# Optimization experiments

Measured on AMD Instinct MI355X. Metric: run time of the kernel, lower is better.

Reference implementation:

```python
import jax, jax.numpy as jnp
import numpy as np

SOS_TOKEN = 1


def gru_cell(x, h, Wih, Whh, bih, bhh):
    # torch.nn.GRU gate math; x:[B,H], h:[B,H]; Wih/Whh:[3H,H]
    gi = x @ Wih.T + bih
    gh = h @ Whh.T + bhh
    ir, iz, inn = jnp.split(gi, 3, axis=-1)
    hr, hz, hn = jnp.split(gh, 3, axis=-1)
    r = jax.nn.sigmoid(ir + hr)
    z = jax.nn.sigmoid(iz + hz)
    n = jnp.tanh(inn + r * hn)
    return (1.0 - z) * n + z * h


def setup_inputs() -> dict:
    key = jax.random.key(0)
    ks = jax.random.split(key, 20)
    B, S, T, V, H = 32, 512, 128, 32000, 512
    sc = 0.08
    p = lambda i, shape: (jax.random.normal(ks[i], shape, jnp.float32) * sc)
    return {
        "input_seq": jax.random.randint(ks[0], (B, S), 0, V),
        "target_seq": jax.random.randint(ks[1], (B, T), 0, V),
        "emb": p(2, (V, H)),
        "ef_Wih": p(3, (3 * H, H)), "ef_Whh": p(4, (3 * H, H)),
        "ef_bih": p(5, (3 * H,)), "ef_bhh": p(6, (3 * H,)),
        "eb_Wih": p(7, (3 * H, H)), "eb_Whh": p(8, (3 * H, H)),
        "eb_bih": p(9, (3 * H,)), "eb_bhh": p(10, (3 * H,)),
        "d_Wih": p(11, (3 * H, H)), "d_Whh": p(12, (3 * H, H)),
        "d_bih": p(13, (3 * H,)), "d_bhh": p(14, (3 * H,)),
        "att_W": p(15, (H, 2 * H)), "att_b": p(16, (H,)),
        "out_W": p(17, (V, H)), "out_b": p(18, (V,)),
    }


def reference(input_seq, target_seq, emb,
              ef_Wih, ef_Whh, ef_bih, ef_bhh,
              eb_Wih, eb_Whh, eb_bih, eb_bhh,
              d_Wih, d_Whh, d_bih, d_bhh,
              att_W, att_b, out_W, out_b):
    B, S = input_seq.shape
    T = target_seq.shape[1]
    H = emb.shape[1]
    dtype = emb.dtype

    # ---- encoder: bidirectional GRU over source ----
    xs = jnp.swapaxes(emb[input_seq], 0, 1)  # [S,B,H]
    h0 = jnp.zeros((B, H), dtype)

    def make_step(Wih, Whh, bih, bhh):
        def f(h, xt):
            hn = gru_cell(xt, h, Wih, Whh, bih, bhh)
            return hn, hn
        return f

    hf_last, out_f = jax.lax.scan(make_step(ef_Wih, ef_Whh, ef_bih, ef_bhh), h0, xs)
    hb_last, out_bwd = jax.lax.scan(make_step(eb_Wih, eb_Whh, eb_bih, eb_bhh), h0, xs[::-1])
    out_bwd = out_bwd[::-1]
    # encoder_output[:, :H] + encoder_output[:, H:]  == sum of directions
    enc_out = jnp.swapaxes(out_f + out_bwd, 0, 1)  # [B,S,H]
    # decoder_hidden = encoder_hidden[-1,0] + encoder_hidden[-1,1]
    h_dec0 = hf_last + hb_last  # [B,H]

    # ---- greedy decode for T steps with argmax feedback ----
    tgt = target_seq.T  # [T,B]
    tok0 = jnp.full((B,), SOS_TOKEN, target_seq.dtype)
    batch_idx = jnp.arange(B)

    def dec_step(carry, tgt_t):
        h, tok, loss = carry
        xt = emb[tok]                                   # [B,H]
        hn = gru_cell(xt, h, d_Wih, d_Whh, d_bih, d_bhh)
        scores = jnp.einsum('bh,bsh->bs', hn, enc_out)  # dot attention
        w = jax.nn.softmax(scores, axis=-1)
        ctx = jnp.einsum('bs,bsh->bh', w, enc_out)
        att_out = jnp.tanh(jnp.concatenate([ctx, hn], axis=-1) @ att_W.T + att_b)
        logits = att_out @ out_W.T + out_b              # [B,V]
        logp = jax.nn.log_softmax(logits, axis=-1)
        loss = loss - logp[batch_idx, tgt_t]            # -log softmax(output)[target]
        nxt = jnp.argmax(logits, axis=-1).astype(tok.dtype)
        return (hn, nxt, loss), None

    init = (h_dec0, tok0, jnp.zeros((B,), dtype))
    (_, _, loss), _ = jax.lax.scan(dec_step, init, tgt)
    # mean over examples of (per-example loss / decoding_cnt)
    return jnp.mean(loss / T)
```

## Files before the change

kernel.cpp:

```cpp
#include <hip/hip_runtime.h>
#include <math.h>

#define B 32
#define S 512
#define T 128
#define V 32000
#define H 512
#define NB 256
#define NTE 512
#define NTD 256
#define LCHUNK 250
#define LROWS 128
#define XPITCH 520

__device__ __forceinline__ float dot4(float acc, float4 a, float4 b){
    return fmaf(a.x,b.x, fmaf(a.y,b.y, fmaf(a.z,b.z, fmaf(a.w,b.w, acc))));
}
__device__ __forceinline__ float sigmoidf_(float x){ return 1.0f/(1.0f+expf(-x)); }

template<int GRPSZ>
__device__ __forceinline__ void gbar_arrive(unsigned* bb, unsigned grp, unsigned n){
    __syncthreads();
    if (threadIdx.x == 0){
        const unsigned r = __hip_atomic_fetch_add(bb + grp*32, 1u,
                              __ATOMIC_RELEASE, __HIP_MEMORY_SCOPE_AGENT);
        if (r == n*(unsigned)GRPSZ - 1u){
            const unsigned q = __hip_atomic_fetch_add(bb + 256, 1u,
                                  __ATOMIC_RELEASE, __HIP_MEMORY_SCOPE_AGENT);
            if (q == n*8u - 1u)
                __hip_atomic_store(bb + 288, n,
                                   __ATOMIC_RELEASE, __HIP_MEMORY_SCOPE_AGENT);
        }
    }
}
__device__ __forceinline__ void gbar_wait(unsigned* bb, unsigned n){
    if (threadIdx.x == 0){
        long guard = 0;
        while (__hip_atomic_load(bb + 288, __ATOMIC_RELAXED, __HIP_MEMORY_SCOPE_AGENT) < n){
            __builtin_amdgcn_s_sleep(2);
            if (++guard > 200000000L) break;
        }
        (void)__hip_atomic_load(bb + 288, __ATOMIC_ACQUIRE, __HIP_MEMORY_SCOPE_AGENT);
    }
    __syncthreads();
}

__global__ __launch_bounds__(NTE, 1) void enc_persistent(
    const int* __restrict__ input_seq, const float* __restrict__ emb,
    const float* __restrict__ fWih, const float* __restrict__ fWhh,
    const float* __restrict__ fbih, const float* __restrict__ fbhh,
    const float* __restrict__ bWih, const float* __restrict__ bWhh,
    const float* __restrict__ bbih, const float* __restrict__ bbhh,
    float* enc_out, float* out_b, unsigned* bars)
{
    __shared__ float wlds[24*512];
    __shared__ float shp[3*128*6];
    __shared__ float xh[32*XPITCH];
    const int bk = blockIdx.x, tid = threadIdx.x;
    const int dir = bk & 1, jg = bk >> 1;
    const int b = tid & 31, jj = (tid>>5)&3, kh = tid>>7;
    const int j = jg*4 + jj;
    const unsigned grp = ((unsigned)jg) & 7u;

    const float *Wih = dir? bWih : fWih;
    const float *Whh = dir? bWhh : fWhh;
    const float *bih = dir? bbih : fbih;
    const float *bhh = dir? bbhh : fbhh;
    float* outp = dir? out_b : enc_out;
    unsigned* bar = bars + dir*1024;

    for (int r=0;r<24;r++){
        const int jr = jg*4 + (r/6);
        const int g  = r % 6;
        const float* src = (g<3) ? (Wih + ((size_t)g*H + jr)*H)
                                 : (Whh + ((size_t)(g-3)*H + jr)*H);
        for (int k=tid;k<H;k+=NTE) wlds[r*512+k] = src[k];
    }
    __syncthreads();

    const float4* wx0 = (const float4*)(wlds + (jj*6+0)*512 + kh*128);
    const float4* wx1 = (const float4*)(wlds + (jj*6+1)*512 + kh*128);
    const float4* wx2 = (const float4*)(wlds + (jj*6+2)*512 + kh*128);
    const float4* wh0 = (const float4*)(wlds + (jj*6+3)*512 + kh*128);
    const float4* wh1 = (const float4*)(wlds + (jj*6+4)*512 + kh*128);
    const float4* wh2 = (const float4*)(wlds + (jj*6+5)*512 + kh*128);
    const float bi_r = bih[j], bi_z = bih[H+j], bi_n = bih[2*H+j];
    const float bh_r = bhh[j], bh_z = bhh[H+j], bh_n = bhh[2*H+j];

    for (int t=0; t<S; t++){
        const int pos  = dir ? (S-1-t) : t;
        const int hpos = dir ? (S-t)   : (t-1);

        #pragma unroll
        for (int it=0; it<8; ++it){
            const int idx = it*NTE + tid;
            const int bb = idx >> 7, c = idx & 127;
            const int tok = input_seq[bb*S + pos];
            ((float4*)(xh + bb*XPITCH))[c] =
                ((const float4*)(emb + (size_t)tok*H))[c];
        }
        __syncthreads();

        float ir=0.f, iz=0.f, in_=0.f;
        {
            const float4* x4 = (const float4*)(xh + b*XPITCH + kh*128);
            #pragma unroll 8
            for (int k=0;k<32;k++){
                const float4 xv = x4[k];
                ir  = dot4(ir , xv, wx0[k]);
                iz  = dot4(iz , xv, wx1[k]);
                in_ = dot4(in_, xv, wx2[k]);
            }
        }

        if (t > 0) gbar_wait(bar, (unsigned)t);

        float hr=0.f, hz=0.f, hn=0.f, hprev = 0.f;
        if (t > 0){
            #pragma unroll
            for (int it=0; it<8; ++it){
                const int idx = it*NTE + tid;
                const int bb = idx >> 7, c = idx & 127;
                ((float4*)(xh + bb*XPITCH))[c] =
                    ((const float4*)(outp + ((size_t)bb*S + hpos)*H))[c];
            }
            __syncthreads();
            const float4* h4 = (const float4*)(xh + b*XPITCH + kh*128);
            #pragma unroll 8
            for (int k=0;k<32;k++){
                const float4 hv = h4[k];
                hr = dot4(hr, hv, wh0[k]);
                hz = dot4(hz, hv, wh1[k]);
                hn = dot4(hn, hv, wh2[k]);
            }
            hprev = xh[b*XPITCH + j];
        }
        if (kh){
            float* p = shp + ((kh-1)*128 + jj*32 + b)*6;
            p[0]=ir; p[1]=iz; p[2]=in_; p[3]=hr; p[4]=hz; p[5]=hn;
        }
        __syncthreads();
        if (!kh){
            #pragma unroll
            for (int q=0;q<3;q++){
                const float* p = shp + (q*128 + jj*32 + b)*6;
                ir+=p[0]; iz+=p[1]; in_+=p[2]; hr+=p[3]; hz+=p[4]; hn+=p[5];
            }
            const float r = sigmoidf_(ir + bi_r + hr + bh_r);
            const float z = sigmoidf_(iz + bi_z + hz + bh_z);
            const float n = tanhf(in_ + bi_n + r*(hn + bh_n));
            outp[((size_t)b*S + pos)*H + j] = (1.0f - z)*n + z*hprev;
        }
        gbar_arrive<16>(bar, grp, (unsigned)(t+1));
    }
}

__global__ __launch_bounds__(NTD, 1) void dec_persistent(
    const int* __restrict__ target_seq, const float* __restrict__ emb,
    const float* __restrict__ dWih, const float* __restrict__ dWhh,
    const float* __restrict__ dbih, const float* __restrict__ dbhh,
    const float* __restrict__ attW, const float* __restrict__ attb,
    const float* __restrict__ outW, const float* __restrict__ outBias,
    float* enc_out, const float* out_b,
    float* hdec, float* scores, float* ctxb, float* att_out,
    float* pm, float* ps, int* pidx, float* lossb,
    float* out, unsigned* bar)
{
    __shared__ __align__(16) float smem[128*33*4];
    __shared__ float wg[12*512];
    __shared__ float wp[2*1024];
    __shared__ float red_m[4][32], red_s[4][32];
    __shared__ int   red_i[4][32];
    __shared__ int sh_tok[B];
    const int bk = blockIdx.x, tid = threadIdx.x;
    const unsigned grp = (unsigned)bk & 7u;
    unsigned bn = 1;
#define GSYNC() do { gbar_arrive<32>(bar, grp, bn); gbar_wait(bar, bn); ++bn; } while(0)

    for (int r=0;r<12;r++){
        const int jr = bk*2 + (r/6);
        const int g  = r % 6;
        const float* src = (g<3) ? (dWih + ((size_t)g*H + jr)*H)
                                 : (dWhh + ((size_t)(g-3)*H + jr)*H);
        for (int k=tid;k<H;k+=NTD) wg[r*512+k] = src[k];
    }
    for (int r=0;r<2;r++){
        const float* src = attW + (size_t)(bk*2+r)*(2*H);
        for (int k=tid;k<2*H;k+=NTD) wp[r*1024+k] = src[k];
    }

    {
        const int gid = bk*NTD + tid;
        if (gid < B*H){
            const int bb = gid >> 9, jq = gid & 511;
            hdec[gid] = enc_out[((size_t)bb*S + (S-1))*H + jq] + out_b[((size_t)bb*S)*H + jq];
        }
        if (bk==0 && tid<B) lossb[tid] = 0.0f;
    }
    GSYNC();

    {
        float4* e4 = (float4*)enc_out; const float4* o4 = (const float4*)out_b;
        for (size_t i = (size_t)bk*NTD + tid; i < (size_t)B*S*H/4; i += (size_t)NB*NTD){
            float4 x = e4[i]; const float4 y = o4[i];
            x.x+=y.x; x.y+=y.y; x.z+=y.z; x.w+=y.w; e4[i]=x;
        }
    }
    GSYNC();

    const int gb = tid & 31, gj = (tid>>5)&1, gkq = tid>>6;
    const int jrow = bk*2 + gj;
    const float4* gwir = (const float4*)(wg + (gj*6+0)*512 + gkq*128);
    const float4* gwiz = (const float4*)(wg + (gj*6+1)*512 + gkq*128);
    const float4* gwin = (const float4*)(wg + (gj*6+2)*512 + gkq*128);
    const float4* gwhr = (const float4*)(wg + (gj*6+3)*512 + gkq*128);
    const float4* gwhz = (const float4*)(wg + (gj*6+4)*512 + gkq*128);
    const float4* gwhn = (const float4*)(wg + (gj*6+5)*512 + gkq*128);
    const float gbi_r = dbih[jrow], gbi_z = dbih[H+jrow], gbi_n = dbih[2*H+jrow];
    const float gbh_r = dbhh[jrow], gbh_z = dbhh[H+jrow], gbh_n = dbhh[2*H+jrow];
    const float4* pw = (const float4*)(wp + gj*1024 + gkq*256);

    for (int t=0; t<T; t++){
        float* hin  = hdec + (size_t)(t&1)*B*H;
        float* hout = hdec + (size_t)((t+1)&1)*B*H;

        if (t == 0){
            if (tid < B) sh_tok[tid] = 1;
        } else {
            const int mb = tid>>3, p = tid&7;
            float bv = -INFINITY; int ai = 0x7FFFFFFF;
            for (int c=p; c<LCHUNK; c+=8){
                const float v = pm[mb*LCHUNK + c];
                if (v > bv){ bv = v; ai = pidx[mb*LCHUNK + c]; }
            }
            #pragma unroll
            for (int m=1; m<8; m<<=1){
                const float ov = __shfl_xor(bv, m); const int oi = __shfl_xor(ai, m);
                if (ov > bv || (ov == bv && oi < ai)){ bv = ov; ai = oi; }
            }
            if (p==0) sh_tok[mb] = ai;
            if (bk == 0){
                float mm = -INFINITY;
                for (int c=p; c<LCHUNK; c+=8) mm = fmaxf(mm, pm[mb*LCHUNK+c]);
                #pragma unroll
                for (int m=1;m<8;m<<=1) mm = fmaxf(mm, __shfl_xor(mm, m));
                float se = 0.0f;
                for (int c=p; c<LCHUNK; c+=8) se += ps[mb*LCHUNK+c]*expf(pm[mb*LCHUNK+c]-mm);
                #pragma unroll
                for (int m=1;m<8;m<<=1) se += __shfl_xor(se, m);
                const int tg = target_seq[mb*T + (t-1)];
                const float4* ar = (const float4*)(att_out + (size_t)mb*H) + p*16;
                const float4* wr = (const float4*)(outW + (size_t)tg*H) + p*16;
                float d = 0.0f;
                #pragma unroll
                for (int k=0;k<16;k++) d = dot4(d, ar[k], wr[k]);
                #pragma unroll
                for (int m=1;m<8;m<<=1) d += __shfl_xor(d, m);
                if (p==0) lossb[mb] += (mm + logf(se)) - (d + outBias[tg]);
            }
        }
        __syncthreads();
        {
            const int tokb = sh_tok[gb];
            const float4* x4 = (const float4*)(emb + (size_t)tokb*H + gkq*128);
            const float4* h4 = (const float4*)(hin + (size_t)gb*H + gkq*128);
            float ir=0.f, iz=0.f, in_=0.f, hr=0.f, hz=0.f, hn=0.f;
            #pragma unroll 4
            for (int k=0;k<32;k++){
                const float4 xv = x4[k], hv = h4[k];
                ir  = dot4(ir , xv, gwir[k]);
                iz  = dot4(iz , xv, gwiz[k]);
                in_ = dot4(in_, xv, gwin[k]);
                hr  = dot4(hr , hv, gwhr[k]);
                hz  = dot4(hz , hv, gwhz[k]);
                hn  = dot4(hn , hv, gwhn[k]);
            }
            if (gkq){
                float* pp = smem + ((gkq-1)*64 + gj*32 + gb)*6;
                pp[0]=ir; pp[1]=iz; pp[2]=in_; pp[3]=hr; pp[4]=hz; pp[5]=hn;
            }
            __syncthreads();
            if (!gkq){
                #pragma unroll
                for (int q=0;q<3;q++){
                    const float* pp = smem + (q*64 + gj*32 + gb)*6;
                    ir+=pp[0]; iz+=pp[1]; in_+=pp[2]; hr+=pp[3]; hz+=pp[4]; hn+=pp[5];
                }
                const float r = sigmoidf_(ir + gbi_r + hr + gbh_r);
                const float z = sigmoidf_(iz + gbi_z + hz + gbh_z);
                const float n = tanhf(in_ + gbi_n + r*(hn + gbh_n));
                const float hprev = hin[(size_t)gb*H + jrow];
                hout[(size_t)gb*H + jrow] = (1.0f - z)*n + z*hprev;
            }
        }
        GSYNC();

        {
            const int bS = bk & 31, sg = bk >> 5;
            if (tid < 128)
                ((float4*)smem)[tid] = ((const float4*)(hout + (size_t)bS*H))[tid];
            __syncthreads();
            const int w = tid >> 6, lane = tid & 63;
            const float4 h0 = ((const float4*)smem)[lane];
            const float4 h1 = ((const float4*)smem)[64 + lane];
            const int sbase = sg*64 + w*16;
            #pragma unroll 4
            for (int i=0;i<16;i+=2){
                const int sA = sbase + i, sB = sA + 1;
                const float4* eA = (const float4*)(enc_out + ((size_t)bS*S + sA)*H);
                const float4* eB = (const float4*)(enc_out + ((size_t)bS*S + sB)*H);
                const float4 a0 = eA[lane], a1 = eA[64+lane];
                const float4 b0 = eB[lane], b1 = eB[64+lane];
                float a = dot4(dot4(0.f, a0, h0), a1, h1);
                float b = dot4(dot4(0.f, b0, h0), b1, h1);
                #pragma unroll
                for (int m=1;m<64;m<<=1){ a += __shfl_xor(a, m); b += __shfl_xor(b, m); }
                if (lane == 0){ scores[bS*S + sA] = a; scores[bS*S + sB] = b; }
            }
        }
        GSYNC();

        {
            const int bC = bk & 31, cg = bk >> 5;
            float* sh_w = smem; float* red = smem + 512; float* part = smem + 768;
            const float s0 = scores[bC*S + tid], s1 = scores[bC*S + tid + 256];
            red[tid] = fmaxf(s0,s1); __syncthreads();
            for (int off=128; off>0; off>>=1){ if (tid<off) red[tid]=fmaxf(red[tid],red[tid+off]); __syncthreads(); }
            const float M = red[0]; __syncthreads();
            const float e0 = expf(s0-M), e1 = expf(s1-M);
            red[tid] = e0+e1; __syncthreads();
            for (int off=128; off>0; off>>=1){ if (tid<off) red[tid]+=red[tid+off]; __syncthreads(); }
            const float inv = 1.0f/red[0];
            __syncthreads();
            sh_w[tid] = e0*inv; sh_w[tid+256] = e1*inv;
            __syncthreads();
            const int col = cg*64 + (tid & 63);
            const int sg2 = tid >> 6;
            const float* Ec = enc_out + (size_t)bC*S*H + col;
            float ac0=0.f, ac1=0.f, ac2=0.f, ac3=0.f;
            #pragma unroll 4
            for (int i=0;i<128;i+=4){
                const int sA = sg2 + 4*i, sB = sA+4, sC = sA+8, sD = sA+12;
                const float vA = Ec[(size_t)sA*H], vB = Ec[(size_t)sB*H];
                const float vC = Ec[(size_t)sC*H], vD = Ec[(size_t)sD*H];
                ac0 = fmaf(sh_w[sA], vA, ac0);
                ac1 = fmaf(sh_w[sB], vB, ac1);
                ac2 = fmaf(sh_w[sC], vC, ac2);
                ac3 = fmaf(sh_w[sD], vD, ac3);
            }
            part[tid] = (ac0+ac1)+(ac2+ac3); __syncthreads();
            if (tid < 64) ctxb[bC*512 + col] = part[tid]+part[tid+64]+part[tid+128]+part[tid+192];
        }
        GSYNC();

        {
            const float* act = (gkq < 2) ? (ctxb + (size_t)gb*512 + gkq*256)
                                         : (hout + (size_t)gb*H + (gkq-2)*256);
            const float4* a4 = (const float4*)act;
            float acc = 0.f;
            #pragma unroll 8
            for (int k=0;k<64;k++) acc = dot4(acc, a4[k], pw[k]);
            if (gkq){
                smem[(gkq-1)*64 + gj*32 + gb] = acc;
            }
            __syncthreads();
            if (!gkq){
                acc += smem[0*64 + gj*32 + gb] + smem[1*64 + gj*32 + gb] + smem[2*64 + gj*32 + gb];
                att_out[(size_t)gb*H + jrow] = tanhf(acc + attb[jrow]);
            }
        }
        GSYNC();

        if (bk < LCHUNK){
            float4* sh4 = (float4*)smem;
            for (int idx = tid; idx < 32*128; idx += NTD){
                const int k4 = idx & 127, bb = idx >> 7;
                sh4[k4*33 + bb] = ((const float4*)att_out)[(size_t)bb*128 + k4];
            }
            __syncthreads();
            const int wid = tid >> 6, lane = tid & 63;
            const int rl = lane & 7, bl = lane >> 3;
            const int r0 = bk*LROWS + wid*32 + rl*4;
            const float4* w0 = (const float4*)(outW + (size_t)(r0+0)*H);
            const float4* w1 = (const float4*)(outW + (size_t)(r0+1)*H);
            const float4* w2 = (const float4*)(outW + (size_t)(r0+2)*H);
            const float4* w3 = (const float4*)(outW + (size_t)(r0+3)*H);
            float acc[4][4];
            #pragma unroll
            for (int i=0;i<4;i++){ acc[i][0]=0.f; acc[i][1]=0.f; acc[i][2]=0.f; acc[i][3]=0.f; }

            float4 A0[4],A1[4],A2[4],A3[4], B0[4],B1[4],B2[4],B3[4];
            #pragma unroll
            for (int kk=0;kk<4;kk++){ A0[kk]=w0[kk]; A1[kk]=w1[kk]; A2[kk]=w2[kk]; A3[kk]=w3[kk]; }
            for (int kc=0; kc<16; kc++){
                const int kbB = kc*8 + 4;
                #pragma unroll
                for (int kk=0;kk<4;kk++){ B0[kk]=w0[kbB+kk]; B1[kk]=w1[kbB+kk]; B2[kk]=w2[kbB+kk]; B3[kk]=w3[kbB+kk]; }
                #pragma unroll
                for (int kk=0;kk<4;kk++){
                    const int k = kc*8 + kk;
                    const float4 a0 = sh4[k*33 + bl*4 + 0];
                    const float4 a1 = sh4[k*33 + bl*4 + 1];
                    const float4 a2 = sh4[k*33 + bl*4 + 2];
                    const float4 a3 = sh4[k*33 + bl*4 + 3];
                    acc[0][0]=dot4(acc[0][0],A0[kk],a0); acc[0][1]=dot4(acc[0][1],A0[kk],a1);
                    acc[0][2]=dot4(acc[0][2],A0[kk],a2); acc[0][3]=dot4(acc[0][3],A0[kk],a3);
                    acc[1][0]=dot4(acc[1][0],A1[kk],a0); acc[1][1]=dot4(acc[1][1],A1[kk],a1);
                    acc[1][2]=dot4(acc[1][2],A1[kk],a2); acc[1][3]=dot4(acc[1][3],A1[kk],a3);
                    acc[2][0]=dot4(acc[2][0],A2[kk],a0); acc[2][1]=dot4(acc[2][1],A2[kk],a1);
                    acc[2][2]=dot4(acc[2][2],A2[kk],a2); acc[2][3]=dot4(acc[2][3],A2[kk],a3);
                    acc[3][0]=dot4(acc[3][0],A3[kk],a0); acc[3][1]=dot4(acc[3][1],A3[kk],a1);
                    acc[3][2]=dot4(acc[3][2],A3[kk],a2); acc[3][3]=dot4(acc[3][3],A3[kk],a3);
                }
                if (kc < 15){
                    const int kbA = kc*8 + 8;
                    #pragma unroll
                    for (int kk=0;kk<4;kk++){ A0[kk]=w0[kbA+kk]; A1[kk]=w1[kbA+kk]; A2[kk]=w2[kbA+kk]; A3[kk]=w3[kbA+kk]; }
                }
                #pragma unroll
                for (int kk=0;kk<4;kk++){
                    const int k = kc*8 + 4 + kk;
                    const float4 a0 = sh4[k*33 + bl*4 + 0];
                    const float4 a1 = sh4[k*33 + bl*4 + 1];
                    const float4 a2 = sh4[k*33 + bl*4 + 2];
                    const float4 a3 = sh4[k*33 + bl*4 + 3];
                    acc[0][0]=dot4(acc[0][0],B0[kk],a0); acc[0][1]=dot4(acc[0][1],B0[kk],a1);
                    acc[0][2]=dot4(acc[0][2],B0[kk],a2); acc[0][3]=dot4(acc[0][3],B0[kk],a3);
                    acc[1][0]=dot4(acc[1][0],B1[kk],a0); acc[1][1]=dot4(acc[1][1],B1[kk],a1);
                    acc[1][2]=dot4(acc[1][2],B1[kk],a2); acc[1][3]=dot4(acc[1][3],B1[kk],a3);
                    acc[2][0]=dot4(acc[2][0],B2[kk],a0); acc[2][1]=dot4(acc[2][1],B2[kk],a1);
                    acc[2][2]=dot4(acc[2][2],B2[kk],a2); acc[2][3]=dot4(acc[2][3],B2[kk],a3);
                    acc[3][0]=dot4(acc[3][0],B3[kk],a0); acc[3][1]=dot4(acc[3][1],B3[kk],a1);
                    acc[3][2]=dot4(acc[3][2],B3[kk],a2); acc[3][3]=dot4(acc[3][3],B3[kk],a3);
                }
            }

            const float bs0 = outBias[r0], bs1 = outBias[r0+1], bs2 = outBias[r0+2], bs3 = outBias[r0+3];
            #pragma unroll
            for (int j=0;j<4;j++){
                const float l0 = acc[0][j]+bs0, l1 = acc[1][j]+bs1, l2 = acc[2][j]+bs2, l3 = acc[3][j]+bs3;
                float M = l0; int bi = r0;
                if (l1 > M){ M=l1; bi=r0+1; }
                if (l2 > M){ M=l2; bi=r0+2; }
                if (l3 > M){ M=l3; bi=r0+3; }
                float Ssum = expf(l0-M)+expf(l1-M)+expf(l2-M)+expf(l3-M);
                #pragma unroll
                for (int m=1;m<8;m<<=1){
                    const float oM = __shfl_xor(M, m);
                    const float oS = __shfl_xor(Ssum, m);
                    const int   oI = __shfl_xor(bi, m);
                    const float nM = fmaxf(M, oM);
                    const float nS = Ssum*expf(M-nM) + oS*expf(oM-nM);
                    if (oM > M || (oM == M && oI < bi)) bi = oI;
                    M = nM; Ssum = nS;
                }
                if (rl == 0){
                    red_m[wid][bl*4+j] = M;
                    red_s[wid][bl*4+j] = Ssum;
                    red_i[wid][bl*4+j] = bi;
                }
            }
            __syncthreads();
            if (tid < 32){
                float M = red_m[0][tid], Ssum = red_s[0][tid]; int bi = red_i[0][tid];
                #pragma unroll
                for (int w=1; w<4; w++){
                    const float oM = red_m[w][tid], oS = red_s[w][tid]; const int oI = red_i[w][tid];
                    const float nM = fmaxf(M, oM);
                    const float nS = Ssum*expf(M-nM) + oS*expf(oM-nM);
                    if (oM > M || (oM == M && oI < bi)) bi = oI;
                    M = nM; Ssum = nS;
                }
                pm[tid*LCHUNK + bk] = M;
                ps[tid*LCHUNK + bk] = Ssum;
                pidx[tid*LCHUNK + bk] = bi;
            }
        }
        GSYNC();
    }

    if (bk == 0){
        const int mb = tid>>3, p = tid&7;
        float mm = -INFINITY;
        for (int c=p; c<LCHUNK; c+=8) mm = fmaxf(mm, pm[mb*LCHUNK+c]);
        #pragma unroll
        for (int m=1;m<8;m<<=1) mm = fmaxf(mm, __shfl_xor(mm, m));
        float se = 0.0f;
        for (int c=p; c<LCHUNK; c+=8) se += ps[mb*LCHUNK+c]*expf(pm[mb*LCHUNK+c]-mm);
        #pragma unroll
        for (int m=1;m<8;m<<=1) se += __shfl_xor(se, m);
        const int tg = target_seq[mb*T + (T-1)];
        const float4* ar = (const float4*)(att_out + (size_t)mb*H) + p*16;
        const float4* wr = (const float4*)(outW + (size_t)tg*H) + p*16;
        float d = 0.0f;
        #pragma unroll
        for (int k=0;k<16;k++) d = dot4(d, ar[k], wr[k]);
        #pragma unroll
        for (int m=1;m<8;m<<=1) d += __shfl_xor(d, m);
        if (p==0) lossb[mb] += (mm + logf(se)) - (d + outBias[tg]);
        __syncthreads();
        if (tid < B){
            float v = lossb[tid];
            for (int off=16; off>0; off>>=1) v += __shfl_down(v, off);
            if (tid == 0) out[0] = v / (float)(B*T);
        }
    }
#undef GSYNC
}

extern "C" void kernel_launch(void* const* d_in, const int* in_sizes, int n_in,
                              void* d_out, int out_size, void* d_ws, size_t ws_size,
                              hipStream_t stream)
{
    const int*   input_seq  = (const int*)  d_in[0];
    const int*   target_seq = (const int*)  d_in[1];
    const float* emb    = (const float*)d_in[2];
    const float* efWih  = (const float*)d_in[3];
    const float* efWhh  = (const float*)d_in[4];
    const float* efbih  = (const float*)d_in[5];
    const float* efbhh  = (const float*)d_in[6];
    const float* ebWih  = (const float*)d_in[7];
    const float* ebWhh  = (const float*)d_in[8];
    const float* ebbih  = (const float*)d_in[9];
    const float* ebbhh  = (const float*)d_in[10];
    const float* dWih   = (const float*)d_in[11];
    const float* dWhh   = (const float*)d_in[12];
    const float* dbih   = (const float*)d_in[13];
    const float* dbhh   = (const float*)d_in[14];
    const float* attW   = (const float*)d_in[15];
    const float* attb   = (const float*)d_in[16];
    const float* outW   = (const float*)d_in[17];
    const float* outBias= (const float*)d_in[18];

    float* ws      = (float*)d_ws;
    unsigned* bars = (unsigned*)ws;
    float* enc_out = ws + 4096;
    float* outb    = enc_out + (size_t)B*S*H;
    float* scores  = outb    + (size_t)B*S*H;
    float* ctxb    = scores  + (size_t)B*S;
    float* attout  = ctxb    + (size_t)B*512;
    float* pm      = attout  + (size_t)B*H;
    float* ps      = pm      + (size_t)B*LCHUNK;
    int*   pidx    = (int*)(ps + (size_t)B*LCHUNK);
    float* hdec    = (float*)(pidx + (size_t)B*LCHUNK);
    float* lossb   = hdec    + (size_t)2*B*H;

    hipMemsetAsync(bars, 0, 16384, stream);

    enc_persistent<<<NB, NTE, 0, stream>>>(input_seq, emb,
        efWih, efWhh, efbih, efbhh, ebWih, ebWhh, ebbih, ebbhh,
        enc_out, outb, bars);

    dec_persistent<<<NB, NTD, 0, stream>>>(target_seq, emb,
        dWih, dWhh, dbih, dbhh, attW, attb, outW, outBias,
        enc_out, outb, hdec, scores, ctxb, attout,
        pm, ps, pidx, lossb, (float*)d_out, bars + 2048);
}
```

Measured before the change: 28.79 ms.

## Double decoder block size to 512 threads and re-partition every phase

Raises the persistent decoder kernel from 256 to 512 threads per block. Each phase (GRU gate dot products, attention scores, softmax/context, attention projection, output-vocab logits) is re-split so every thread does half the K-range or half the rows, with wider shared-memory reductions. The aim is more in-flight memory requests and latency hiding per CU in a latency-bound, barrier-heavy persistent loop. In exchange it adds longer reduction chains and costs more registers per CU.

```diff
diff --git a/kernel.cpp b/kernel.cpp
--- a/kernel.cpp
+++ b/kernel.cpp
@@ -8,7 +8,7 @@
 #define H 512
 #define NB 256
 #define NTE 512
-#define NTD 256
+#define NTD 512
 #define LCHUNK 250
 #define LROWS 128
 #define XPITCH 520
@@ -169,8 +169,8 @@
     __shared__ __align__(16) float smem[128*33*4];
     __shared__ float wg[12*512];
     __shared__ float wp[2*1024];
-    __shared__ float red_m[4][32], red_s[4][32];
-    __shared__ int   red_i[4][32];
+    __shared__ float red_m[8][32], red_s[8][32];
+    __shared__ int   red_i[8][32];
     __shared__ int sh_tok[B];
     const int bk = blockIdx.x, tid = threadIdx.x;
     const unsigned grp = (unsigned)bk & 7u;
@@ -210,15 +210,15 @@
 
     const int gb = tid & 31, gj = (tid>>5)&1, gkq = tid>>6;
     const int jrow = bk*2 + gj;
-    const float4* gwir = (const float4*)(wg + (gj*6+0)*512 + gkq*128);
-    const float4* gwiz = (const float4*)(wg + (gj*6+1)*512 + gkq*128);
-    const float4* gwin = (const float4*)(wg + (gj*6+2)*512 + gkq*128);
-    const float4* gwhr = (const float4*)(wg + (gj*6+3)*512 + gkq*128);
-    const float4* gwhz = (const float4*)(wg + (gj*6+4)*512 + gkq*128);
-    const float4* gwhn = (const float4*)(wg + (gj*6+5)*512 + gkq*128);
+    const float4* gwir = (const float4*)(wg + (gj*6+0)*512 + gkq*64);
+    const float4* gwiz = (const float4*)(wg + (gj*6+1)*512 + gkq*64);
+    const float4* gwin = (const float4*)(wg + (gj*6+2)*512 + gkq*64);
+    const float4* gwhr = (const float4*)(wg + (gj*6+3)*512 + gkq*64);
+    const float4* gwhz = (const float4*)(wg + (gj*6+4)*512 + gkq*64);
+    const float4* gwhn = (const float4*)(wg + (gj*6+5)*512 + gkq*64);
     const float gbi_r = dbih[jrow], gbi_z = dbih[H+jrow], gbi_n = dbih[2*H+jrow];
     const float gbh_r = dbhh[jrow], gbh_z = dbhh[H+jrow], gbh_n = dbhh[2*H+jrow];
-    const float4* pw = (const float4*)(wp + gj*1024 + gkq*256);
+    const float4* pw = (const float4*)(wp + gj*1024 + gkq*128);
 
     for (int t=0; t<T; t++){
         float* hin  = hdec + (size_t)(t&1)*B*H;
@@ -226,7 +226,7 @@
 
         if (t == 0){
             if (tid < B) sh_tok[tid] = 1;
-        } else {
+        } else if (tid < 256) {
             const int mb = tid>>3, p = tid&7;
             float bv = -INFINITY; int ai = 0x7FFFFFFF;
             for (int c=p; c<LCHUNK; c+=8){
@@ -262,11 +262,11 @@
         __syncthreads();
         {
             const int tokb = sh_tok[gb];
-            const float4* x4 = (const float4*)(emb + (size_t)tokb*H + gkq*128);
-            const float4* h4 = (const float4*)(hin + (size_t)gb*H + gkq*128);
+            const float4* x4 = (const float4*)(emb + (size_t)tokb*H + gkq*64);
+            const float4* h4 = (const float4*)(hin + (size_t)gb*H + gkq*64);
             float ir=0.f, iz=0.f, in_=0.f, hr=0.f, hz=0.f, hn=0.f;
-            #pragma unroll 4
-            for (int k=0;k<32;k++){
+            #pragma unroll
+            for (int k=0;k<16;k++){
                 const float4 xv = x4[k], hv = h4[k];
                 ir  = dot4(ir , xv, gwir[k]);
                 iz  = dot4(iz , xv, gwiz[k]);
@@ -282,7 +282,7 @@
             __syncthreads();
             if (!gkq){
                 #pragma unroll
-                for (int q=0;q<3;q++){
+                for (int q=0;q<7;q++){
                     const float* pp = smem + (q*64 + gj*32 + gb)*6;
                     ir+=pp[0]; iz+=pp[1]; in_+=pp[2]; hr+=pp[3]; hz+=pp[4]; hn+=pp[5];
                 }
@@ -303,9 +303,9 @@
             const int w = tid >> 6, lane = tid & 63;
             const float4 h0 = ((const float4*)smem)[lane];
             const float4 h1 = ((const float4*)smem)[64 + lane];
-            const int sbase = sg*64 + w*16;
-            #pragma unroll 4
-            for (int i=0;i<16;i+=2){
+            const int sbase = sg*64 + w*8;
+            #pragma unroll
+            for (int i=0;i<8;i+=2){
                 const int sA = sbase + i, sB = sA + 1;
                 const float4* eA = (const float4*)(enc_out + ((size_t)bS*S + sA)*H);
                 const float4* eB = (const float4*)(enc_out + ((size_t)bS*S + sB)*H);
@@ -322,25 +322,25 @@
 
         {
             const int bC = bk & 31, cg = bk >> 5;
-            float* sh_w = smem; float* red = smem + 512; float* part = smem + 768;
-            const float s0 = scores[bC*S + tid], s1 = scores[bC*S + tid + 256];
-            red[tid] = fmaxf(s0,s1); __syncthreads();
-            for (int off=128; off>0; off>>=1){ if (tid<off) red[tid]=fmaxf(red[tid],red[tid+off]); __syncthreads(); }
+            float* sh_w = smem; float* red = smem + 512; float* part = smem + 1024;
+            const float s0 = scores[bC*S + tid];
+            red[tid] = s0; __syncthreads();
+            for (int off=256; off>0; off>>=1){ if (tid<off) red[tid]=fmaxf(red[tid],red[tid+off]); __syncthreads(); }
             const float M = red[0]; __syncthreads();
-            const float e0 = expf(s0-M), e1 = expf(s1-M);
-            red[tid] = e0+e1; __syncthreads();
-            for (int off=128; off>0; off>>=1){ if (tid<off) red[tid]+=red[tid+off]; __syncthreads(); }
+            const float e0 = expf(s0-M);
+            red[tid] = e0; __syncthreads();
+            for (int off=256; off>0; off>>=1){ if (tid<off) red[tid]+=red[tid+off]; __syncthreads(); }
             const float inv = 1.0f/red[0];
             __syncthreads();
-            sh_w[tid] = e0*inv; sh_w[tid+256] = e1*inv;
+            sh_w[tid] = e0*inv;
             __syncthreads();
             const int col = cg*64 + (tid & 63);
             const int sg2 = tid >> 6;
             const float* Ec = enc_out + (size_t)bC*S*H + col;
             float ac0=0.f, ac1=0.f, ac2=0.f, ac3=0.f;
             #pragma unroll 4
-            for (int i=0;i<128;i+=4){
-                const int sA = sg2 + 4*i, sB = sA+4, sC = sA+8, sD = sA+12;
+            for (int i=0;i<64;i+=4){
+                const int sA = sg2 + 8*i, sB = sA+8, sC = sA+16, sD = sA+24;
                 const float vA = Ec[(size_t)sA*H], vB = Ec[(size_t)sB*H];
                 const float vC = Ec[(size_t)sC*H], vD = Ec[(size_t)sD*H];
                 ac0 = fmaf(sh_w[sA], vA, ac0);
@@ -349,23 +349,29 @@
                 ac3 = fmaf(sh_w[sD], vD, ac3);
             }
             part[tid] = (ac0+ac1)+(ac2+ac3); __syncthreads();
-            if (tid < 64) ctxb[bC*512 + col] = part[tid]+part[tid+64]+part[tid+128]+part[tid+192];
+            if (tid < 64){
+                float v = 0.f;
+                #pragma unroll
+                for (int i=0;i<8;i++) v += part[tid + 64*i];
+                ctxb[bC*512 + cg*64 + tid] = v;
+            }
         }
         GSYNC();
 
         {
-            const float* act = (gkq < 2) ? (ctxb + (size_t)gb*512 + gkq*256)
-                                         : (hout + (size_t)gb*H + (gkq-2)*256);
+            const float* act = (gkq < 4) ? (ctxb + (size_t)gb*512 + gkq*128)
+                                         : (hout + (size_t)gb*H + (gkq-4)*128);
             const float4* a4 = (const float4*)act;
             float acc = 0.f;
-            #pragma unroll 8
-            for (int k=0;k<64;k++) acc = dot4(acc, a4[k], pw[k]);
+            #pragma unroll
+            for (int k=0;k<32;k++) acc = dot4(acc, a4[k], pw[k]);
             if (gkq){
                 smem[(gkq-1)*64 + gj*32 + gb] = acc;
             }
             __syncthreads();
             if (!gkq){
-                acc += smem[0*64 + gj*32 + gb] + smem[1*64 + gj*32 + gb] + smem[2*64 + gj*32 + gb];
+                #pragma unroll
+                for (int q=0;q<7;q++) acc += smem[q*64 + gj*32 + gb];
                 att_out[(size_t)gb*H + jrow] = tanhf(acc + attb[jrow]);
             }
         }
@@ -380,22 +386,20 @@
             __syncthreads();
             const int wid = tid >> 6, lane = tid & 63;
             const int rl = lane & 7, bl = lane >> 3;
-            const int r0 = bk*LROWS + wid*32 + rl*4;
+            const int r0 = bk*LROWS + wid*16 + rl*2;
             const float4* w0 = (const float4*)(outW + (size_t)(r0+0)*H);
             const float4* w1 = (const float4*)(outW + (size_t)(r0+1)*H);
-            const float4* w2 = (const float4*)(outW + (size_t)(r0+2)*H);
-            const float4* w3 = (const float4*)(outW + (size_t)(r0+3)*H);
-            float acc[4][4];
-            #pragma unroll
-            for (int i=0;i<4;i++){ acc[i][0]=0.f; acc[i][1]=0.f; acc[i][2]=0.f; acc[i][3]=0.f; }
-
-            float4 A0[4],A1[4],A2[4],A3[4], B0[4],B1[4],B2[4],B3[4];
-            #pragma unroll
-            for (int kk=0;kk<4;kk++){ A0[kk]=w0[kk]; A1[kk]=w1[kk]; A2[kk]=w2[kk]; A3[kk]=w3[kk]; }
+            float acc[2][4];
+            acc[0][0]=0.f; acc[0][1]=0.f; acc[0][2]=0.f; acc[0][3]=0.f;
+            acc[1][0]=0.f; acc[1][1]=0.f; acc[1][2]=0.f; acc[1][3]=0.f;
+
+            float4 A0[4],A1[4], B0[4],B1[4];
+            #pragma unroll
+            for (int kk=0;kk<4;kk++){ A0[kk]=w0[kk]; A1[kk]=w1[kk]; }
             for (int kc=0; kc<16; kc++){
                 const int kbB = kc*8 + 4;
                 #pragma unroll
-                for (int kk=0;kk<4;kk++){ B0[kk]=w0[kbB+kk]; B1[kk]=w1[kbB+kk]; B2[kk]=w2[kbB+kk]; B3[kk]=w3[kbB+kk]; }
+                for (int kk=0;kk<4;kk++){ B0[kk]=w0[kbB+kk]; B1[kk]=w1[kbB+kk]; }
                 #pragma unroll
                 for (int kk=0;kk<4;kk++){
                     const int k = kc*8 + kk;
@@ -407,15 +411,11 @@
                     acc[0][2]=dot4(acc[0][2],A0[kk],a2); acc[0][3]=dot4(acc[0][3],A0[kk],a3);
                     acc[1][0]=dot4(acc[1][0],A1[kk],a0); acc[1][1]=dot4(acc[1][1],A1[kk],a1);
                     acc[1][2]=dot4(acc[1][2],A1[kk],a2); acc[1][3]=dot4(acc[1][3],A1[kk],a3);
-                    acc[2][0]=dot4(acc[2][0],A2[kk],a0); acc[2][1]=dot4(acc[2][1],A2[kk],a1);
-                    acc[2][2]=dot4(acc[2][2],A2[kk],a2); acc[2][3]=dot4(acc[2][3],A2[kk],a3);
-                    acc[3][0]=dot4(acc[3][0],A3[kk],a0); acc[3][1]=dot4(acc[3][1],A3[kk],a1);
-                    acc[3][2]=dot4(acc[3][2],A3[kk],a2); acc[3][3]=dot4(acc[3][3],A3[kk],a3);
                 }
                 if (kc < 15){
                     const int kbA = kc*8 + 8;
                     #pragma unroll
-                    for (int kk=0;kk<4;kk++){ A0[kk]=w0[kbA+kk]; A1[kk]=w1[kbA+kk]; A2[kk]=w2[kbA+kk]; A3[kk]=w3[kbA+kk]; }
+                    for (int kk=0;kk<4;kk++){ A0[kk]=w0[kbA+kk]; A1[kk]=w1[kbA+kk]; }
                 }
                 #pragma unroll
                 for (int kk=0;kk<4;kk++){
@@ -428,22 +428,16 @@
                     acc[0][2]=dot4(acc[0][2],B0[kk],a2); acc[0][3]=dot4(acc[0][3],B0[kk],a3);
                     acc[1][0]=dot4(acc[1][0],B1[kk],a0); acc[1][1]=dot4(acc[1][1],B1[kk],a1);
                     acc[1][2]=dot4(acc[1][2],B1[kk],a2); acc[1][3]=dot4(acc[1][3],B1[kk],a3);
-                    acc[2][0]=dot4(acc[2][0],B2[kk],a0); acc[2][1]=dot4(acc[2][1],B2[kk],a1);
-                    acc[2][2]=dot4(acc[2][2],B2[kk],a2); acc[2][3]=dot4(acc[2][3],B2[kk],a3);
-                    acc[3][0]=dot4(acc[3][0],B3[kk],a0); acc[3][1]=dot4(acc[3][1],B3[kk],a1);
-                    acc[3][2]=dot4(acc[3][2],B3[kk],a2); acc[3][3]=dot4(acc[3][3],B3[kk],a3);
-                }
-            }
-
-            const float bs0 = outBias[r0], bs1 = outBias[r0+1], bs2 = outBias[r0+2], bs3 = outBias[r0+3];
+                }
+            }
+
+            const float bs0 = outBias[r0], bs1 = outBias[r0+1];
             #pragma unroll
             for (int j=0;j<4;j++){
-                const float l0 = acc[0][j]+bs0, l1 = acc[1][j]+bs1, l2 = acc[2][j]+bs2, l3 = acc[3][j]+bs3;
+                const float l0 = acc[0][j]+bs0, l1 = acc[1][j]+bs1;
                 float M = l0; int bi = r0;
                 if (l1 > M){ M=l1; bi=r0+1; }
-                if (l2 > M){ M=l2; bi=r0+2; }
-                if (l3 > M){ M=l3; bi=r0+3; }
-                float Ssum = expf(l0-M)+expf(l1-M)+expf(l2-M)+expf(l3-M);
+                float Ssum = expf(l0-M)+expf(l1-M);
                 #pragma unroll
                 for (int m=1;m<8;m<<=1){
                     const float oM = __shfl_xor(M, m);
@@ -464,7 +458,7 @@
             if (tid < 32){
                 float M = red_m[0][tid], Ssum = red_s[0][tid]; int bi = red_i[0][tid];
                 #pragma unroll
-                for (int w=1; w<4; w++){
+                for (int w=1; w<8; w++){
                     const float oM = red_m[w][tid], oS = red_s[w][tid]; const int oI = red_i[w][tid];
                     const float nM = fmaxf(M, oM);
                     const float nS = Ssum*expf(M-nM) + oS*expf(oM-nM);
@@ -480,24 +474,26 @@
     }
 
     if (bk == 0){
-        const int mb = tid>>3, p = tid&7;
-        float mm = -INFINITY;
-        for (int c=p; c<LCHUNK; c+=8) mm = fmaxf(mm, pm[mb*LCHUNK+c]);
-        #pragma unroll
-        for (int m=1;m<8;m<<=1) mm = fmaxf(mm, __shfl_xor(mm, m));
-        float se = 0.0f;
-        for (int c=p; c<LCHUNK; c+=8) se += ps[mb*LCHUNK+c]*expf(pm[mb*LCHUNK+c]-mm);
-        #pragma unroll
-        for (int m=1;m<8;m<<=1) se += __shfl_xor(se, m);
-        const int tg = target_seq[mb*T + (T-1)];
-        const float4* ar = (const float4*)(att_out + (size_t)mb*H) + p*16;
-        const float4* wr = (const float4*)(outW + (size_t)tg*H) + p*16;
-        float d = 0.0f;
-        #pragma unroll
-        for (int k=0;k<16;k++) d = dot4(d, ar[k], wr[k]);
-        #pragma unroll
-        for (int m=1;m<8;m<<=1) d += __shfl_xor(d, m);
-        if (p==0) lossb[mb] += (mm + logf(se)) - (d + outBias[tg]);
+        if (tid < 256){
+            const int mb = tid>>3, p = tid&7;
+            float mm = -INFINITY;
+            for (int c=p; c<LCHUNK; c+=8) mm = fmaxf(mm, pm[mb*LCHUNK+c]);
+            #pragma unroll
+            for (int m=1;m<8;m<<=1) mm = fmaxf(mm, __shfl_xor(mm, m));
+            float se = 0.0f;
+            for (int c=p; c<LCHUNK; c+=8) se += ps[mb*LCHUNK+c]*expf(pm[mb*LCHUNK+c]-mm);
+            #pragma unroll
+            for (int m=1;m<8;m<<=1) se += __shfl_xor(se, m);
+            const int tg = target_seq[mb*T + (T-1)];
+            const float4* ar = (const float4*)(att_out + (size_t)mb*H) + p*16;
+            const float4* wr = (const float4*)(outW + (size_t)tg*H) + p*16;
+            float d = 0.0f;
+            #pragma unroll
+            for (int k=0;k<16;k++) d = dot4(d, ar[k], wr[k]);
+            #pragma unroll
+            for (int m=1;m<8;m<<=1) d += __shfl_xor(d, m);
+            if (p==0) lossb[mb] += (mm + logf(se)) - (d + outBias[tg]);
+        }
         __syncthreads();
         if (tid < B){
             float v = lossb[tid];
```

New measurement: 30.20 ms. 1.05x slower.

## Pin a quarter of each block's output-projection weights in LDS

Applied to the files above, without the earlier changes.

Each decoder block now preloads the first 32 of its 128 output-projection rows into shared memory once, and wave 0 reads them from LDS every step while the other waves keep streaming from global memory. To free LDS, the attention-projection weights are no longer cached and are read from global memory each step. The per-batch loss reduction is also spread across blocks (bk==mb) instead of all running in block 0. This trades less global/L2 traffic for the big vocab GEMV against extra global reads for the attention weights and load imbalance between waves.

```diff
diff --git a/kernel.cpp b/kernel.cpp
--- a/kernel.cpp
+++ b/kernel.cpp
@@ -11,6 +11,8 @@
 #define NTD 256
 #define LCHUNK 250
 #define LROWS 128
+#define NPIN 32
+#define PINP 516
 #define XPITCH 520
 
 __device__ __forceinline__ float dot4(float acc, float4 a, float4 b){
@@ -168,7 +170,7 @@
 {
     __shared__ __align__(16) float smem[128*33*4];
     __shared__ float wg[12*512];
-    __shared__ float wp[2*1024];
+    __shared__ __align__(16) float pinw[NPIN*PINP];
     __shared__ float red_m[4][32], red_s[4][32];
     __shared__ int   red_i[4][32];
     __shared__ int sh_tok[B];
@@ -184,9 +186,12 @@
                                  : (dWhh + ((size_t)(g-3)*H + jr)*H);
         for (int k=tid;k<H;k+=NTD) wg[r*512+k] = src[k];
     }
-    for (int r=0;r<2;r++){
-        const float* src = attW + (size_t)(bk*2+r)*(2*H);
-        for (int k=tid;k<2*H;k+=NTD) wp[r*1024+k] = src[k];
+    if (bk < LCHUNK){
+        for (int idx = tid; idx < NPIN*128; idx += NTD){
+            const int row = idx >> 7, k4 = idx & 127;
+            ((float4*)(pinw + row*PINP))[k4] =
+                ((const float4*)(outW + (size_t)(bk*LROWS + row)*H))[k4];
+        }
     }
 
     {
@@ -218,7 +223,7 @@
     const float4* gwhn = (const float4*)(wg + (gj*6+5)*512 + gkq*128);
     const float gbi_r = dbih[jrow], gbi_z = dbih[H+jrow], gbi_n = dbih[2*H+jrow];
     const float gbh_r = dbhh[jrow], gbh_z = dbhh[H+jrow], gbh_n = dbhh[2*H+jrow];
-    const float4* pw = (const float4*)(wp + gj*1024 + gkq*256);
+    const float4* pwG = (const float4*)(attW + (size_t)jrow*(2*H)) + gkq*64;
 
     for (int t=0; t<T; t++){
         float* hin  = hdec + (size_t)(t&1)*B*H;
@@ -239,7 +244,7 @@
                 if (ov > bv || (ov == bv && oi < ai)){ bv = ov; ai = oi; }
             }
             if (p==0) sh_tok[mb] = ai;
-            if (bk == 0){
+            if (bk == mb){
                 float mm = -INFINITY;
                 for (int c=p; c<LCHUNK; c+=8) mm = fmaxf(mm, pm[mb*LCHUNK+c]);
                 #pragma unroll
@@ -359,7 +364,7 @@
             const float4* a4 = (const float4*)act;
             float acc = 0.f;
             #pragma unroll 8
-            for (int k=0;k<64;k++) acc = dot4(acc, a4[k], pw[k]);
+            for (int k=0;k<64;k++) acc = dot4(acc, a4[k], pwG[k]);
             if (gkq){
                 smem[(gkq-1)*64 + gj*32 + gb] = acc;
             }
@@ -381,57 +386,83 @@
             const int wid = tid >> 6, lane = tid & 63;
             const int rl = lane & 7, bl = lane >> 3;
             const int r0 = bk*LROWS + wid*32 + rl*4;
-            const float4* w0 = (const float4*)(outW + (size_t)(r0+0)*H);
-            const float4* w1 = (const float4*)(outW + (size_t)(r0+1)*H);
-            const float4* w2 = (const float4*)(outW + (size_t)(r0+2)*H);
-            const float4* w3 = (const float4*)(outW + (size_t)(r0+3)*H);
             float acc[4][4];
             #pragma unroll
             for (int i=0;i<4;i++){ acc[i][0]=0.f; acc[i][1]=0.f; acc[i][2]=0.f; acc[i][3]=0.f; }
 
-            float4 A0[4],A1[4],A2[4],A3[4], B0[4],B1[4],B2[4],B3[4];
-            #pragma unroll
-            for (int kk=0;kk<4;kk++){ A0[kk]=w0[kk]; A1[kk]=w1[kk]; A2[kk]=w2[kk]; A3[kk]=w3[kk]; }
-            for (int kc=0; kc<16; kc++){
-                const int kbB = kc*8 + 4;
-                #pragma unroll
-                for (int kk=0;kk<4;kk++){ B0[kk]=w0[kbB+kk]; B1[kk]=w1[kbB+kk]; B2[kk]=w2[kbB+kk]; B3[kk]=w3[kbB+kk]; }
-                #pragma unroll
-                for (int kk=0;kk<4;kk++){
-                    const int k = kc*8 + kk;
+            if (wid == 0){
+                const float4* p0 = (const float4*)(pinw + (rl*4+0)*PINP);
+                const float4* p1 = (const float4*)(pinw + (rl*4+1)*PINP);
+                const float4* p2 = (const float4*)(pinw + (rl*4+2)*PINP);
+                const float4* p3 = (const float4*)(pinw + (rl*4+3)*PINP);
+                #pragma unroll 4
+                for (int k=0;k<128;k++){
                     const float4 a0 = sh4[k*33 + bl*4 + 0];
                     const float4 a1 = sh4[k*33 + bl*4 + 1];
                     const float4 a2 = sh4[k*33 + bl*4 + 2];
                     const float4 a3 = sh4[k*33 + bl*4 + 3];
-                    acc[0][0]=dot4(acc[0][0],A0[kk],a0); acc[0][1]=dot4(acc[0][1],A0[kk],a1);
-                    acc[0][2]=dot4(acc[0][2],A0[kk],a2); acc[0][3]=dot4(acc[0][3],A0[kk],a3);
-                    acc[1][0]=dot4(acc[1][0],A1[kk],a0); acc[1][1]=dot4(acc[1][1],A1[kk],a1);
-                    acc[1][2]=dot4(acc[1][2],A1[kk],a2); acc[1][3]=dot4(acc[1][3],A1[kk],a3);
-                    acc[2][0]=dot4(acc[2][0],A2[kk],a0); acc[2][1]=dot4(acc[2][1],A2[kk],a1);
-                    acc[2][2]=dot4(acc[2][2],A2[kk],a2); acc[2][3]=dot4(acc[2][3],A2[kk],a3);
-                    acc[3][0]=dot4(acc[3][0],A3[kk],a0); acc[3][1]=dot4(acc[3][1],A3[kk],a1);
-                    acc[3][2]=dot4(acc[3][2],A3[kk],a2); acc[3][3]=dot4(acc[3][3],A3[kk],a3);
+                    {   const float4 wv = p0[k];
+                        acc[0][0]=dot4(acc[0][0],wv,a0); acc[0][1]=dot4(acc[0][1],wv,a1);
+                        acc[0][2]=dot4(acc[0][2],wv,a2); acc[0][3]=dot4(acc[0][3],wv,a3); }
+                    {   const float4 wv = p1[k];
+                        acc[1][0]=dot4(acc[1][0],wv,a0); acc[1][1]=dot4(acc[1][1],wv,a1);
+                        acc[1][2]=dot4(acc[1][2],wv,a2); acc[1][3]=dot4(acc[1][3],wv,a3); }
+                    {   const float4 wv = p2[k];
+                        acc[2][0]=dot4(acc[2][0],wv,a0); acc[2][1]=dot4(acc[2][1],wv,a1);
+                        acc[2][2]=dot4(acc[2][2],wv,a2); acc[2][3]=dot4(acc[2][3],wv,a3); }
+                    {   const float4 wv = p3[k];
+                        acc[3][0]=dot4(acc[3][0],wv,a0); acc[3][1]=dot4(acc[3][1],wv,a1);
+                        acc[3][2]=dot4(acc[3][2],wv,a2); acc[3][3]=dot4(acc[3][3],wv,a3); }
                 }
-                if (kc < 15){
-                    const int kbA = kc*8 + 8;
+            } else {
+                const float4* w0 = (const float4*)(outW + (size_t)(r0+0)*H);
+                const float4* w1 = (const float4*)(outW + (size_t)(r0+1)*H);
+                const float4* w2 = (const float4*)(outW + (size_t)(r0+2)*H);
+                const float4* w3 = (const float4*)(outW + (size_t)(r0+3)*H);
+                float4 A0[4],A1[4],A2[4],A3[4], B0[4],B1[4],B2[4],B3[4];
+                #pragma unroll
+                for (int kk=0;kk<4;kk++){ A0[kk]=w0[kk]; A1[kk]=w1[kk]; A2[kk]=w2[kk]; A3[kk]=w3[kk]; }
+                for (int kc=0; kc<16; kc++){
+                    const int kbB = kc*8 + 4;
                     #pragma unroll
-                    for (int kk=0;kk<4;kk++){ A0[kk]=w0[kbA+kk]; A1[kk]=w1[kbA+kk]; A2[kk]=w2[kbA+kk]; A3[kk]=w3[kbA+kk]; }
-                }
-                #pragma unroll
-                for (int kk=0;kk<4;kk++){
-                    const int k = kc*8 + 4 + kk;
-                    const float4 a0 = sh4[k*33 + bl*4 + 0];
-                    const float4 a1 = sh4[k*33 + bl*4 + 1];
-                    const float4 a2 = sh4[k*33 + bl*4 + 2];
-                    const float4 a3 = sh4[k*33 + bl*4 + 3];
-                    acc[0][0]=dot4(acc[0][0],B0[kk],a0); acc[0][1]=dot4(acc[0][1],B0[kk],a1);
-                    acc[0][2]=dot4(acc[0][2],B0[kk],a2); acc[0][3]=dot4(acc[0][3],B0[kk],a3);
-                    acc[1][0]=dot4(acc[1][0],B1[kk],a0); acc[1][1]=dot4(acc[1][1],B1[kk],a1);
-                    acc[1][2]=dot4(acc[1][2],B1[kk],a2); acc[1][3]=dot4(acc[1][3],B1[kk],a3);
-                    acc[2][0]=dot4(acc[2][0],B2[kk],a0); acc[2][1]=dot4(acc[2][1],B2[kk],a1);
-                    acc[2][2]=dot4(acc[2][2],B2[kk],a2); acc[2][3]=dot4(acc[2][3],B2[kk],a3);
-                    acc[3][0]=dot4(acc[3][0],B3[kk],a0); acc[3][1]=dot4(acc[3][1],B3[kk],a1);
-                    acc[3][2]=dot4(acc[3][2],B3[kk],a2); acc[3][3]=dot4(acc[3][3],B3[kk],a3);
+                    for (int kk=0;kk<4;kk++){ B0[kk]=w0[kbB+kk]; B1[kk]=w1[kbB+kk]; B2[kk]=w2[kbB+kk]; B3[kk]=w3[kbB+kk]; }
+                    #pragma unroll
+                    for (int kk=0;kk<4;kk++){
+                        const int k = kc*8 + kk;
+                        const float4 a0 = sh4[k*33 + bl*4 + 0];
+                        const float4 a1 = sh4[k*33 + bl*4 + 1];
+                        const float4 a2 = sh4[k*33 + bl*4 + 2];
+                        const float4 a3 = sh4[k*33 + bl*4 + 3];
+                        acc[0][0]=dot4(acc[0][0],A0[kk],a0); acc[0][1]=dot4(acc[0][1],A0[kk],a1);
+                        acc[0][2]=dot4(acc[0][2],A0[kk],a2); acc[0][3]=dot4(acc[0][3],A0[kk],a3);
+                        acc[1][0]=dot4(acc[1][0],A1[kk],a0); acc[1][1]=dot4(acc[1][1],A1[kk],a1);
+                        acc[1][2]=dot4(acc[1][2],A1[kk],a2); acc[1][3]=dot4(acc[1][3],A1[kk],a3);
+                        acc[2][0]=dot4(acc[2][0],A2[kk],a0); acc[2][1]=dot4(acc[2][1],A2[kk],a1);
+                        acc[2][2]=dot4(acc[2][2],A2[kk],a2); acc[2][3]=dot4(acc[2][3],A2[kk],a3);
+                        acc[3][0]=dot4(acc[3][0],A3[kk],a0); acc[3][1]=dot4(acc[3][1],A3[kk],a1);
+                        acc[3][2]=dot4(acc[3][2],A3[kk],a2); acc[3][3]=dot4(acc[3][3],A3[kk],a3);
+                    }
+                    if (kc < 15){
+                        const int kbA = kc*8 + 8;
+                        #pragma unroll
+                        for (int kk=0;kk<4;kk++){ A0[kk]=w0[kbA+kk]; A1[kk]=w1[kbA+kk]; A2[kk]=w2[kbA+kk]; A3[kk]=w3[kbA+kk]; }
+                    }
+                    #pragma unroll
+                    for (int kk=0;kk<4;kk++){
+                        const int k = kc*8 + 4 + kk;
+                        const float4 a0 = sh4[k*33 + bl*4 + 0];
+                        const float4 a1 = sh4[k*33 + bl*4 + 1];
+                        const float4 a2 = sh4[k*33 + bl*4 + 2];
+                        const float4 a3 = sh4[k*33 + bl*4 + 3];
+                        acc[0][0]=dot4(acc[0][0],B0[kk],a0); acc[0][1]=dot4(acc[0][1],B0[kk],a1);
+                        acc[0][2]=dot4(acc[0][2],B0[kk],a2); acc[0][3]=dot4(acc[0][3],B0[kk],a3);
+                        acc[1][0]=dot4(acc[1][0],B1[kk],a0); acc[1][1]=dot4(acc[1][1],B1[kk],a1);
+                        acc[1][2]=dot4(acc[1][2],B1[kk],a2); acc[1][3]=dot4(acc[1][3],B1[kk],a3);
+                        acc[2][0]=dot4(acc[2][0],B2[kk],a0); acc[2][1]=dot4(acc[2][1],B2[kk],a1);
+                        acc[2][2]=dot4(acc[2][2],B2[kk],a2); acc[2][3]=dot4(acc[2][3],B2[kk],a3);
+                        acc[3][0]=dot4(acc[3][0],B3[kk],a0); acc[3][1]=dot4(acc[3][1],B3[kk],a1);
+                        acc[3][2]=dot4(acc[3][2],B3[kk],a2); acc[3][3]=dot4(acc[3][3],B3[kk],a3);
+                    }
                 }
             }
 
```

Measured after the change: 26.41 ms. 8.2% less time.
